# Optimization experiments

Hardware: AMD Instinct MI355X
Metric: run time of the kernel (lower is better)

The kernel has to match this reference:

```python
import jax, jax.numpy as jnp
import numpy as np

B, S, I, H = 32, 1024, 128, 128
D = 2 * H  # bidirectional concat feature dim


def setup_inputs() -> dict:
    key = jax.random.key(0)
    ks = jax.random.split(key, 12)
    lim = 1.0 / np.sqrt(H)  # PyTorch LSTMCell uniform init bound
    u = lambda k, shape: jax.random.uniform(k, shape, jnp.float32, -lim, lim)
    x = jax.random.normal(ks[0], (B, S, I), jnp.float32)
    return {
        "x": x,
        "fw_Wih": u(ks[1], (4 * H, I)), "fw_Whh": u(ks[2], (4 * H, H)),
        "fw_bih": u(ks[3], (4 * H,)),   "fw_bhh": u(ks[4], (4 * H,)),
        "bw_Wih": u(ks[5], (4 * H, I)), "bw_Whh": u(ks[6], (4 * H, H)),
        "bw_bih": u(ks[7], (4 * H,)),   "bw_bhh": u(ks[8], (4 * H,)),
        "Wq": u(ks[9], (D, D)), "Wk": u(ks[10], (D, D)), "Wv": u(ks[11], (D, D)),
    }


def _lstm_dir(x, Wih, Whh, bih, bhh):
    # x: [B, S, I] -> hidden states [B, S, H]; PyTorch LSTMCell gate math.
    xg = jnp.einsum('bsi,gi->bsg', x, Wih) + bih + bhh  # precompute input projections

    def step(carry, xg_t):
        h, c = carry
        g = xg_t + h @ Whh.T
        i_, f_, g_, o_ = jnp.split(g, 4, axis=-1)
        c = jax.nn.sigmoid(f_) * c + jax.nn.sigmoid(i_) * jnp.tanh(g_)
        h = jax.nn.sigmoid(o_) * jnp.tanh(c)
        return (h, c), h

    h0 = jnp.zeros((x.shape[0], Whh.shape[1]), x.dtype)
    _, hs = jax.lax.scan(step, (h0, h0), jnp.swapaxes(xg, 0, 1))
    return jnp.swapaxes(hs, 0, 1)


def reference(x, fw_Wih, fw_Whh, fw_bih, fw_bhh,
              bw_Wih, bw_Whh, bw_bih, bw_bhh, Wq, Wk, Wv):
    f_h = _lstm_dir(x, fw_Wih, fw_Whh, fw_bih, fw_bhh)            # [B,S,H]
    b_h = _lstm_dir(x[:, ::-1, :], bw_Wih, bw_Whh, bw_bih, bw_bhh)[:, ::-1, :]
    h = jnp.concatenate([f_h, b_h], axis=2)                        # [B,S,2H]
    q = h @ Wq.T
    k = h @ Wk.T
    v = h @ Wv.T
    att = jnp.einsum('bsd,btd->bst', q, k) / jnp.sqrt(jnp.asarray(D, h.dtype))
    att = jax.nn.softmax(att, axis=2)
    return jnp.einsum('bst,btd->bsd', att, v)
```

## Files before the change

kernel.cpp:

```cpp
#include <hip/hip_runtime.h>

typedef unsigned short u16;
typedef unsigned int u32;
typedef __bf16 bf16x8 __attribute__((ext_vector_type(8)));
typedef bf16x8 __attribute__((may_alias)) bf16x8a;
typedef float f32x4 __attribute__((ext_vector_type(4)));
typedef _Float16 f16;
typedef _Float16 f16x2 __attribute__((ext_vector_type(2)));

#define BB 32
#define SS 1024
#define HH 128
#define DD 256

__device__ __forceinline__ float b2f(u16 u) {
    u32 v = ((u32)u) << 16;
    return __builtin_bit_cast(float, v);
}
__device__ __forceinline__ u16 f2b(float f) {
    u32 u = __builtin_bit_cast(u32, f);
    u32 r = (u + 0x7fffu + ((u >> 16) & 1u)) >> 16;
    return (u16)r;
}
__device__ __forceinline__ float sig_fast(float x) {
    return __builtin_amdgcn_rcpf(1.0f + __builtin_amdgcn_exp2f(-1.4426950408889634f * x));
}
__device__ __forceinline__ float tanh_fast(float x) {
    return 2.0f * sig_fast(2.0f * x) - 1.0f;
}
template <int CTRL>
__device__ __forceinline__ float dpp_xor(float x) {
    return __builtin_bit_cast(float,
        __builtin_amdgcn_update_dpp(0, __builtin_bit_cast(int, x),
                                    CTRL, 0xF, 0xF, true));
}
__device__ __forceinline__ void lds_barrier() {
    asm volatile("s_waitcnt lgkmcnt(0)\n\ts_barrier" ::: "memory");
}

__global__ __launch_bounds__(256) void conv_weights(
    const float* __restrict__ fwWih, const float* __restrict__ bwWih,
    const float* __restrict__ fwWhh, const float* __restrict__ bwWhh,
    const float* __restrict__ Wq, const float* __restrict__ Wk,
    const float* __restrict__ Wv,
    u16* __restrict__ wfih, u16* __restrict__ wbih, u16* __restrict__ whhf,
    u16* __restrict__ wq, u16* __restrict__ wk, u16* __restrict__ wv)
{
    const int which = blockIdx.y;
    const float* src; u16* dst; int mode;
    switch (which) {
        case 0: src = fwWih; dst = wfih;              mode = 0; break;
        case 1: src = bwWih; dst = wbih;              mode = 0; break;
        case 2: src = fwWhh; dst = whhf;              mode = 1; break;
        case 3: src = bwWhh; dst = whhf + 512 * 128;  mode = 1; break;
        case 4: src = Wq;    dst = wq;                mode = 2; break;
        case 5: src = Wk;    dst = wk;                mode = 2; break;
        default: src = Wv;   dst = wv;                mode = 2; break;
    }
    for (int i = blockIdx.x * 256 + threadIdx.x; i < 65536 / 4; i += 32 * 256) {
        float4 v = ((const float4*)src)[i];
        ushort4 o;
        if (mode == 1) {
            o.x = __builtin_bit_cast(u16, (f16)v.x);
            o.y = __builtin_bit_cast(u16, (f16)v.y);
            o.z = __builtin_bit_cast(u16, (f16)v.z);
            o.w = __builtin_bit_cast(u16, (f16)v.w);
        } else {
            o.x = f2b(v.x); o.y = f2b(v.y); o.z = f2b(v.z); o.w = f2b(v.w);
        }
        if (mode == 2) {
            ((ushort4*)dst)[i] = o;
        } else {
            int r = i >> 5, c4 = i & 31;
            int rp = ((r & 127) << 2) | (r >> 7);
            *(ushort4*)&dst[rp * 128 + c4 * 4] = o;
        }
    }
}

template <int MODE, int AFP32>
__device__ __forceinline__ void gemm_core(
    const void* __restrict__ Araw, const u16* __restrict__ Bt,
    const float* __restrict__ bias1, const float* __restrict__ bias2,
    u16* __restrict__ Cout, int K, int N)
{
    __shared__ u16 As[128 * 72];
    __shared__ u16 Bs[128 * 72];
    const int tid = threadIdx.x;
    const int lane = tid & 63, wave = tid >> 6;
    const int wm = wave >> 1, wn = wave & 1;
    const int lo = lane & 15, hi = lane >> 4;
    const int m0 = blockIdx.x * 128, n0 = blockIdx.y * 128;

    f32x4 acc[4][4] = {};

    for (int k0 = 0; k0 < K; k0 += 64) {
        __syncthreads();
#pragma unroll
        for (int i = 0; i < 4; i++) {
            int c = tid + 256 * i;
            int row = c >> 3, kc = (c & 7) * 8;
            if (AFP32) {
                const float* ap = (const float*)Araw + (size_t)(m0 + row) * K + k0 + kc;
                float4 v0 = *(const float4*)ap;
                float4 v1 = *(const float4*)(ap + 4);
                uint4 o;
                o.x = (u32)f2b(v0.x) | ((u32)f2b(v0.y) << 16);
                o.y = (u32)f2b(v0.z) | ((u32)f2b(v0.w) << 16);
                o.z = (u32)f2b(v1.x) | ((u32)f2b(v1.y) << 16);
                o.w = (u32)f2b(v1.z) | ((u32)f2b(v1.w) << 16);
                *(uint4*)&As[row * 72 + kc] = o;
            } else {
                *(uint4*)&As[row * 72 + kc] =
                    *(const uint4*)&((const u16*)Araw)[(size_t)(m0 + row) * K + k0 + kc];
            }
            *(uint4*)&Bs[row * 72 + kc] =
                *(const uint4*)&Bt[(size_t)(n0 + row) * K + k0 + kc];
        }
        __syncthreads();
#pragma unroll
        for (int ks = 0; ks < 2; ks++) {
            bf16x8 af[4], bfr[4];
#pragma unroll
            for (int i = 0; i < 4; i++)
                af[i] = *(const bf16x8a*)&As[(wm * 64 + i * 16 + lo) * 72 + ks * 32 + hi * 8];
#pragma unroll
            for (int j = 0; j < 4; j++)
                bfr[j] = *(const bf16x8a*)&Bs[(wn * 64 + j * 16 + lo) * 72 + ks * 32 + hi * 8];
#pragma unroll
            for (int i = 0; i < 4; i++)
#pragma unroll
                for (int j = 0; j < 4; j++)
                    acc[i][j] = __builtin_amdgcn_mfma_f32_16x16x32_bf16(
                        af[i], bfr[j], acc[i][j], 0, 0, 0);
        }
    }
#pragma unroll
    for (int j = 0; j < 4; j++) {
        int col = n0 + wn * 64 + j * 16 + lo;
        float bsum = 0.f;
        if (MODE == 1) {
            int co = ((col & 3) << 7) | (col >> 2);
            bsum = bias1[co] + bias2[co];
        }
#pragma unroll
        for (int i = 0; i < 4; i++) {
            int row0 = m0 + wm * 64 + i * 16 + hi * 4;
#pragma unroll
            for (int r = 0; r < 4; r++) {
                float v = acc[i][j][r] + bsum;
                if (MODE == 1) {
                    int row = row0 + r;
                    int sidx = row & 1023, bidx = row >> 10;
                    Cout[(size_t)sidx * (BB * 512) + bidx * 512 + col] = f2b(v);
                } else {
                    Cout[(size_t)(row0 + r) * N + col] = f2b(v);
                }
            }
        }
    }
}

__global__ __launch_bounds__(256) void gemm_xg(
    const float* __restrict__ A, const u16* __restrict__ Bt_f,
    const u16* __restrict__ Bt_b,
    const float* __restrict__ f_bih, const float* __restrict__ f_bhh,
    const float* __restrict__ b_bih, const float* __restrict__ b_bhh,
    u16* __restrict__ xg)
{
    const int dir = blockIdx.z;
    gemm_core<1, 1>(A, dir ? Bt_b : Bt_f,
                    dir ? b_bih : f_bih, dir ? b_bhh : f_bhh,
                    xg + (size_t)dir * SS * BB * 512, 128, 512);
}

__global__ __launch_bounds__(256) void gemm_qkv(
    const u16* __restrict__ A, const u16* __restrict__ Wq,
    const u16* __restrict__ Wk, const u16* __restrict__ Wv,
    u16* __restrict__ qb, u16* __restrict__ kb, u16* __restrict__ vb)
{
    const int z = blockIdx.z;
    const u16* Bt = (z == 0) ? Wq : (z == 1) ? Wk : Wv;
    u16* out = (z == 0) ? qb : (z == 1) ? kb : vb;
    gemm_core<0, 0>(A, Bt, nullptr, nullptr, out, 256, 256);
}

__global__ __launch_bounds__(256)
__attribute__((amdgpu_waves_per_eu(1, 1)))
void lstm_scan_sk(
    const u16* __restrict__ Whh_h,
    const u16* __restrict__ xg,
    u16* __restrict__ hout)
{
    const int wg = blockIdx.x;
    const int dir = wg >> 5, b = wg & 31;
    const int t_ = threadIdx.x;
    const int u = t_ >> 1;
    const int kh = t_ & 1;

    u32 w[4][32];
    {
        const volatile u32* vp = (const volatile u32*)(Whh_h + (size_t)dir * 512 * 128);
#pragma unroll
        for (int g = 0; g < 4; g++) {
            int base = ((4 * u + g) * 128 + kh * 64) >> 1;
#pragma unroll
            for (int k = 0; k < 32; k++) w[g][k] = vp[base + k];
        }
    }

    __shared__ __align__(16) u16 hbuf[2][128];
    if (t_ < 128) hbuf[0][t_] = 0;
    float c = 0.0f;

    const u16* xgp = xg + (size_t)dir * SS * (BB * 512) + (size_t)b * 512 + 4 * u;
    u16* hop = hout + (size_t)b * SS * DD + dir * HH + u;

    int s = dir ? (SS - 1) : 0;
    const int d1 = dir ? -1 : 1;
    uint2 nxA = *(const uint2*)&xgp[(size_t)s * (BB * 512)];
    uint2 nxB = *(const uint2*)&xgp[(size_t)(s + d1) * (BB * 512)];
    lds_barrier();

    auto body = [&](uint2& nx, int parity) {
        uint2 xv = nx;
        int sp = s + 2 * d1;
        if ((unsigned)sp < SS)
            nx = *(const uint2*)&xgp[(size_t)sp * (BB * 512)];

        const uint4* hb = (const uint4*)&hbuf[parity][kh * 64];
        float g0 = 0.f, g1 = 0.f, g2 = 0.f, g3 = 0.f;
#pragma unroll
        for (int cc = 0; cc < 8; cc++) {
            uint4 hh = hb[cc];
            u32 hv[4] = {hh.x, hh.y, hh.z, hh.w};
#pragma unroll
            for (int j = 0; j < 4; j++) {
                f16x2 hp = __builtin_bit_cast(f16x2, hv[j]);
                g0 = __builtin_amdgcn_fdot2(hp, __builtin_bit_cast(f16x2, w[0][4 * cc + j]), g0, false);
                g1 = __builtin_amdgcn_fdot2(hp, __builtin_bit_cast(f16x2, w[1][4 * cc + j]), g1, false);
                g2 = __builtin_amdgcn_fdot2(hp, __builtin_bit_cast(f16x2, w[2][4 * cc + j]), g2, false);
                g3 = __builtin_amdgcn_fdot2(hp, __builtin_bit_cast(f16x2, w[3][4 * cc + j]), g3, false);
            }
        }
        g0 += dpp_xor<0xB1>(g0);
        g1 += dpp_xor<0xB1>(g1);
        g2 += dpp_xor<0xB1>(g2);
        g3 += dpp_xor<0xB1>(g3);
        g0 += b2f((u16)(xv.x & 0xffff)); g1 += b2f((u16)(xv.x >> 16));
        g2 += b2f((u16)(xv.y & 0xffff)); g3 += b2f((u16)(xv.y >> 16));

        c = fmaf(sig_fast(g1), c, sig_fast(g0) * tanh_fast(g2));
        float h = sig_fast(g3) * tanh_fast(c);

        if (kh == 0)
            hbuf[parity ^ 1][u] = __builtin_bit_cast(u16, (f16)h);
        else
            hop[(size_t)s * DD] = f2b(h);
        lds_barrier();
        s += d1;
    };

    for (int t = 0; t < SS; t += 2) {
        body(nxA, 0);
        body(nxB, 1);
    }
}

__global__ __launch_bounds__(256) void transpose_v(
    const u16* __restrict__ v, u16* __restrict__ vT)
{
    __shared__ u16 tile[64 * 72];
    const int b = blockIdx.z, s0 = blockIdx.x * 64, d0 = blockIdx.y * 64;
    const int tid = threadIdx.x;
#pragma unroll
    for (int i = 0; i < 2; i++) {
        int c = tid + 256 * i;
        int sl = c >> 3, dc = (c & 7) * 8;
        *(uint4*)&tile[sl * 72 + dc] =
            *(const uint4*)&v[((size_t)b * SS + s0 + sl) * DD + d0 + dc];
    }
    __syncthreads();
#pragma unroll
    for (int i = 0; i < 2; i++) {
        int c = tid + 256 * i;
        int dl = c >> 3, sc = (c & 7) * 8;
        u32 x0 = (u32)tile[(sc + 0) * 72 + dl] | ((u32)tile[(sc + 1) * 72 + dl] << 16);
        u32 x1 = (u32)tile[(sc + 2) * 72 + dl] | ((u32)tile[(sc + 3) * 72 + dl] << 16);
        u32 x2 = (u32)tile[(sc + 4) * 72 + dl] | ((u32)tile[(sc + 5) * 72 + dl] << 16);
        u32 x3 = (u32)tile[(sc + 6) * 72 + dl] | ((u32)tile[(sc + 7) * 72 + dl] << 16);
        uint4 val; val.x = x0; val.y = x1; val.z = x2; val.w = x3;
        *(uint4*)&vT[((size_t)b * DD + d0 + dl) * SS + s0 + sc] = val;
    }
}

__global__ __launch_bounds__(256) void attn_kernel(
    const u16* __restrict__ q, const u16* __restrict__ k,
    const u16* __restrict__ vT, float* __restrict__ out)
{
    __shared__ u16 Ks[32 * 264];
    __shared__ u16 Vs[256 * 40];
    __shared__ u16 Ps[64 * 40];
    const int b = blockIdx.y, q0 = blockIdx.x * 64;
    const int tid = threadIdx.x, wave = tid >> 6, lane = tid & 63;
    const int lo = lane & 15, hi = lane >> 4;
    const float c1 = 0.09016844005556021f;

    bf16x8 qf[8];
    {
        const u16* qp = q + ((size_t)b * SS + q0 + wave * 16 + lo) * DD;
#pragma unroll
        for (int ks = 0; ks < 8; ks++)
            qf[ks] = *(const bf16x8a*)&qp[ks * 32 + hi * 8];
    }
    float m_i[4] = {-1e30f, -1e30f, -1e30f, -1e30f};
    float l_i[4] = {0.f, 0.f, 0.f, 0.f};
    f32x4 o[16] = {};

    for (int t0 = 0; t0 < SS; t0 += 32) {
        __syncthreads();
#pragma unroll
        for (int i = 0; i < 4; i++) {
            int c = tid + 256 * i;
            {
                int row = c >> 5, dc = (c & 31) * 8;
                *(uint4*)&Ks[row * 264 + dc] =
                    *(const uint4*)&k[((size_t)b * SS + t0 + row) * DD + dc];
            }
            {
                int d = c >> 2, sc = (c & 3) * 8;
                *(uint4*)&Vs[d * 40 + sc] =
                    *(const uint4*)&vT[((size_t)b * DD + d) * SS + t0 + sc];
            }
        }
        __syncthreads();

        f32x4 sacc[2] = {};
#pragma unroll
        for (int ks = 0; ks < 8; ks++) {
#pragma unroll
            for (int j = 0; j < 2; j++) {
                bf16x8 bfr = *(const bf16x8a*)&Ks[(j * 16 + lo) * 264 + ks * 32 + hi * 8];
                sacc[j] = __builtin_amdgcn_mfma_f32_16x16x32_bf16(qf[ks], bfr, sacc[j], 0, 0, 0);
            }
        }

        float tt[2][4];
#pragma unroll
        for (int j = 0; j < 2; j++)
#pragma unroll
            for (int r = 0; r < 4; r++) tt[j][r] = sacc[j][r] * c1;
        float rm[4];
#pragma unroll
        for (int r = 0; r < 4; r++) rm[r] = fmaxf(tt[0][r], tt[1][r]);
#pragma unroll
        for (int mm = 1; mm <= 8; mm <<= 1)
#pragma unroll
            for (int r = 0; r < 4; r++) rm[r] = fmaxf(rm[r], __shfl_xor(rm[r], mm, 64));
        float al[4], rs[4];
#pragma unroll
        for (int r = 0; r < 4; r++) {
            float mn = fmaxf(m_i[r], rm[r]);
            al[r] = __builtin_amdgcn_exp2f(m_i[r] - mn);
            m_i[r] = mn;
            rs[r] = 0.f;
        }
#pragma unroll
        for (int j = 0; j < 2; j++)
#pragma unroll
            for (int r = 0; r < 4; r++) {
                float p = __builtin_amdgcn_exp2f(tt[j][r] - m_i[r]);
                rs[r] += p;
                Ps[(wave * 16 + hi * 4 + r) * 40 + j * 16 + lo] = f2b(p);
            }
#pragma unroll
        for (int mm = 1; mm <= 8; mm <<= 1)
#pragma unroll
            for (int r = 0; r < 4; r++) rs[r] += __shfl_xor(rs[r], mm, 64);
#pragma unroll
        for (int r = 0; r < 4; r++) l_i[r] = l_i[r] * al[r] + rs[r];
#pragma unroll
        for (int nt = 0; nt < 16; nt++) {
            o[nt][0] *= al[0]; o[nt][1] *= al[1];
            o[nt][2] *= al[2]; o[nt][3] *= al[3];
        }
        __syncthreads();
        bf16x8 pa = *(const bf16x8a*)&Ps[(wave * 16 + lo) * 40 + hi * 8];
#pragma unroll
        for (int nt = 0; nt < 16; nt++) {
            bf16x8 bv = *(const bf16x8a*)&Vs[(nt * 16 + lo) * 40 + hi * 8];
            o[nt] = __builtin_amdgcn_mfma_f32_16x16x32_bf16(pa, bv, o[nt], 0, 0, 0);
        }
    }
    float inv[4];
#pragma unroll
    for (int r = 0; r < 4; r++) inv[r] = __builtin_amdgcn_rcpf(l_i[r]);
#pragma unroll
    for (int nt = 0; nt < 16; nt++)
#pragma unroll
        for (int r = 0; r < 4; r++) {
            int row = q0 + wave * 16 + hi * 4 + r;
            int col = nt * 16 + lo;
            out[((size_t)b * SS + row) * DD + col] = o[nt][r] * inv[r];
        }
}

extern "C" void kernel_launch(void* const* d_in, const int* in_sizes, int n_in,
                              void* d_out, int out_size, void* d_ws, size_t ws_size,
                              hipStream_t stream)
{
    (void)in_sizes; (void)n_in; (void)out_size;
    const float* x      = (const float*)d_in[0];
    const float* fw_Wih = (const float*)d_in[1];
    const float* fw_Whh = (const float*)d_in[2];
    const float* fw_bih = (const float*)d_in[3];
    const float* fw_bhh = (const float*)d_in[4];
    const float* bw_Wih = (const float*)d_in[5];
    const float* bw_Whh = (const float*)d_in[6];
    const float* bw_bih = (const float*)d_in[7];
    const float* bw_bhh = (const float*)d_in[8];
    const float* Wq = (const float*)d_in[9];
    const float* Wk = (const float*)d_in[10];
    const float* Wv = (const float*)d_in[11];

    if (ws_size < 143523840ULL) return;

    char* ws = (char*)d_ws;
    u16* xg  = (u16*)ws;
    u16* h   = (u16*)(ws + 67108864);
    u16* qb  = (u16*)(ws + 83886080);
    u16* kb  = (u16*)(ws + 100663296);
    u16* vT  = (u16*)(ws + 117440512);
    u16* wfih16 = (u16*)(ws + 142606336);
    u16* wbih16 = (u16*)(ws + 142606336 + 131072);
    u16* wq16   = (u16*)(ws + 142606336 + 262144);
    u16* wk16   = (u16*)(ws + 142606336 + 393216);
    u16* wv16   = (u16*)(ws + 142606336 + 524288);
    u16* whhf16 = (u16*)(ws + 142606336 + 655360);
    u16* vb = (u16*)ws;

    conv_weights<<<dim3(32, 7), 256, 0, stream>>>(
        fw_Wih, bw_Wih, fw_Whh, bw_Whh, Wq, Wk, Wv,
        wfih16, wbih16, whhf16, wq16, wk16, wv16);

    gemm_xg<<<dim3(256, 4, 2), 256, 0, stream>>>(
        x, wfih16, wbih16, fw_bih, fw_bhh, bw_bih, bw_bhh, xg);
    lstm_scan_sk<<<64, 256, 0, stream>>>(whhf16, xg, h);
    gemm_qkv<<<dim3(256, 2, 3), 256, 0, stream>>>(h, wq16, wk16, wv16, qb, kb, vb);
    transpose_v<<<dim3(16, 4, 32), 256, 0, stream>>>(vb, vT);
    attn_kernel<<<dim3(16, 32), 256, 0, stream>>>(qb, kb, vT, (float*)d_out);
}
```

Before: 765.8 us.

## Process two batch rows per LSTM scan workgroup, halving the grid

Each LSTM scan workgroup now carries two independent batch sequences, reusing the register-resident Whh weights for both dot products and sharing one barrier per timestep. The grid shrinks from 64 to 32 workgroups. The aim is to give the serial, latency-bound recurrence more independent instructions per step to hide latency and to amortise barrier cost. In exchange, each step does twice the arithmetic and register pressure rises, and fewer CUs are used.

Result: slower. 1.150 ms (+50.2%).

```diff
diff --git a/kernel.cpp b/kernel.cpp
--- a/kernel.cpp
+++ b/kernel.cpp
@@ -193,7 +193,9 @@
     u16* __restrict__ hout)
 {
     const int wg = blockIdx.x;
-    const int dir = wg >> 5, b = wg & 31;
+    const int dir = wg >> 4;
+    const int bA = (wg & 15) * 2;
+    const int bB = bA + 1;
     const int t_ = threadIdx.x;
     const int u = t_ >> 1;
     const int kh = t_ & 1;
@@ -209,61 +211,87 @@
         }
     }
 
-    __shared__ __align__(16) u16 hbuf[2][128];
-    if (t_ < 128) hbuf[0][t_] = 0;
-    float c = 0.0f;
-
-    const u16* xgp = xg + (size_t)dir * SS * (BB * 512) + (size_t)b * 512 + 4 * u;
-    u16* hop = hout + (size_t)b * SS * DD + dir * HH + u;
+    __shared__ __align__(16) u16 hbuf[2][2][128];
+    if (t_ < 128) { hbuf[0][0][t_] = 0; hbuf[1][0][t_] = 0; }
+    float cA = 0.0f, cB = 0.0f;
+
+    const u16* xgpA = xg + (size_t)dir * SS * (BB * 512) + (size_t)bA * 512 + 4 * u;
+    const u16* xgpB = xg + (size_t)dir * SS * (BB * 512) + (size_t)bB * 512 + 4 * u;
+    u16* hopA = hout + (size_t)bA * SS * DD + dir * HH + u;
+    u16* hopB = hout + (size_t)bB * SS * DD + dir * HH + u;
 
     int s = dir ? (SS - 1) : 0;
     const int d1 = dir ? -1 : 1;
-    uint2 nxA = *(const uint2*)&xgp[(size_t)s * (BB * 512)];
-    uint2 nxB = *(const uint2*)&xgp[(size_t)(s + d1) * (BB * 512)];
+    uint2 nxA0 = *(const uint2*)&xgpA[(size_t)s * (BB * 512)];
+    uint2 nxB0 = *(const uint2*)&xgpB[(size_t)s * (BB * 512)];
+    uint2 nxA1 = *(const uint2*)&xgpA[(size_t)(s + d1) * (BB * 512)];
+    uint2 nxB1 = *(const uint2*)&xgpB[(size_t)(s + d1) * (BB * 512)];
     lds_barrier();
 
-    auto body = [&](uint2& nx, int parity) {
-        uint2 xv = nx;
+    auto body = [&](uint2& nxa, uint2& nxb, int parity) {
+        uint2 xva = nxa, xvb = nxb;
         int sp = s + 2 * d1;
-        if ((unsigned)sp < SS)
-            nx = *(const uint2*)&xgp[(size_t)sp * (BB * 512)];
-
-        const uint4* hb = (const uint4*)&hbuf[parity][kh * 64];
-        float g0 = 0.f, g1 = 0.f, g2 = 0.f, g3 = 0.f;
+        if ((unsigned)sp < SS) {
+            nxa = *(const uint2*)&xgpA[(size_t)sp * (BB * 512)];
+            nxb = *(const uint2*)&xgpB[(size_t)sp * (BB * 512)];
+        }
+
+        const uint4* hbA = (const uint4*)&hbuf[0][parity][kh * 64];
+        const uint4* hbB = (const uint4*)&hbuf[1][parity][kh * 64];
+        float a0 = 0.f, a1 = 0.f, a2 = 0.f, a3 = 0.f;
+        float b0 = 0.f, b1 = 0.f, b2 = 0.f, b3 = 0.f;
 #pragma unroll
         for (int cc = 0; cc < 8; cc++) {
-            uint4 hh = hb[cc];
-            u32 hv[4] = {hh.x, hh.y, hh.z, hh.w};
+            uint4 hhA = hbA[cc];
+            uint4 hhB = hbB[cc];
+            u32 hvA[4] = {hhA.x, hhA.y, hhA.z, hhA.w};
+            u32 hvB[4] = {hhB.x, hhB.y, hhB.z, hhB.w};
 #pragma unroll
             for (int j = 0; j < 4; j++) {
-                f16x2 hp = __builtin_bit_cast(f16x2, hv[j]);
-                g0 = __builtin_amdgcn_fdot2(hp, __builtin_bit_cast(f16x2, w[0][4 * cc + j]), g0, false);
-                g1 = __builtin_amdgcn_fdot2(hp, __builtin_bit_cast(f16x2, w[1][4 * cc + j]), g1, false);
-                g2 = __builtin_amdgcn_fdot2(hp, __builtin_bit_cast(f16x2, w[2][4 * cc + j]), g2, false);
-                g3 = __builtin_amdgcn_fdot2(hp, __builtin_bit_cast(f16x2, w[3][4 * cc + j]), g3, false);
-            }
-        }
-        g0 += dpp_xor<0xB1>(g0);
-        g1 += dpp_xor<0xB1>(g1);
-        g2 += dpp_xor<0xB1>(g2);
-        g3 += dpp_xor<0xB1>(g3);
-        g0 += b2f((u16)(xv.x & 0xffff)); g1 += b2f((u16)(xv.x >> 16));
-        g2 += b2f((u16)(xv.y & 0xffff)); g3 += b2f((u16)(xv.y >> 16));
-
-        c = fmaf(sig_fast(g1), c, sig_fast(g0) * tanh_fast(g2));
-        float h = sig_fast(g3) * tanh_fast(c);
-
-        if (kh == 0)
-            hbuf[parity ^ 1][u] = __builtin_bit_cast(u16, (f16)h);
-        else
-            hop[(size_t)s * DD] = f2b(h);
+                f16x2 wp0 = __builtin_bit_cast(f16x2, w[0][4 * cc + j]);
+                f16x2 wp1 = __builtin_bit_cast(f16x2, w[1][4 * cc + j]);
+                f16x2 wp2 = __builtin_bit_cast(f16x2, w[2][4 * cc + j]);
+                f16x2 wp3 = __builtin_bit_cast(f16x2, w[3][4 * cc + j]);
+                f16x2 hpA = __builtin_bit_cast(f16x2, hvA[j]);
+                f16x2 hpB = __builtin_bit_cast(f16x2, hvB[j]);
+                a0 = __builtin_amdgcn_fdot2(hpA, wp0, a0, false);
+                b0 = __builtin_amdgcn_fdot2(hpB, wp0, b0, false);
+                a1 = __builtin_amdgcn_fdot2(hpA, wp1, a1, false);
+                b1 = __builtin_amdgcn_fdot2(hpB, wp1, b1, false);
+                a2 = __builtin_amdgcn_fdot2(hpA, wp2, a2, false);
+                b2 = __builtin_amdgcn_fdot2(hpB, wp2, b2, false);
+                a3 = __builtin_amdgcn_fdot2(hpA, wp3, a3, false);
+                b3 = __builtin_amdgcn_fdot2(hpB, wp3, b3, false);
+            }
+        }
+        a0 += dpp_xor<0xB1>(a0); b0 += dpp_xor<0xB1>(b0);
+        a1 += dpp_xor<0xB1>(a1); b1 += dpp_xor<0xB1>(b1);
+        a2 += dpp_xor<0xB1>(a2); b2 += dpp_xor<0xB1>(b2);
+        a3 += dpp_xor<0xB1>(a3); b3 += dpp_xor<0xB1>(b3);
+        a0 += b2f((u16)(xva.x & 0xffff)); a1 += b2f((u16)(xva.x >> 16));
+        a2 += b2f((u16)(xva.y & 0xffff)); a3 += b2f((u16)(xva.y >> 16));
+        b0 += b2f((u16)(xvb.x & 0xffff)); b1 += b2f((u16)(xvb.x >> 16));
+        b2 += b2f((u16)(xvb.y & 0xffff)); b3 += b2f((u16)(xvb.y >> 16));
+
+        cA = fmaf(sig_fast(a1), cA, sig_fast(a0) * tanh_fast(a2));
+        cB = fmaf(sig_fast(b1), cB, sig_fast(b0) * tanh_fast(b2));
+        float hA = sig_fast(a3) * tanh_fast(cA);
+        float hB = sig_fast(b3) * tanh_fast(cB);
+
+        if (kh == 0) {
+            hbuf[0][parity ^ 1][u] = __builtin_bit_cast(u16, (f16)hA);
+            hbuf[1][parity ^ 1][u] = __builtin_bit_cast(u16, (f16)hB);
+        } else {
+            hopA[(size_t)s * DD] = f2b(hA);
+            hopB[(size_t)s * DD] = f2b(hB);
+        }
         lds_barrier();
         s += d1;
     };
 
     for (int t = 0; t < SS; t += 2) {
-        body(nxA, 0);
-        body(nxB, 1);
+        body(nxA0, nxB0, 0);
+        body(nxA1, nxB1, 1);
     }
 }
 
@@ -445,7 +473,7 @@
 
     gemm_xg<<<dim3(256, 4, 2), 256, 0, stream>>>(
         x, wfih16, wbih16, fw_bih, fw_bhh, bw_bih, bw_bhh, xg);
-    lstm_scan_sk<<<64, 256, 0, stream>>>(whhf16, xg, h);
+    lstm_scan_sk<<<32, 256, 0, stream>>>(whhf16, xg, h);
     gemm_qkv<<<dim3(256, 2, 3), 256, 0, stream>>>(h, wq16, wk16, wv16, qb, kb, vb);
     transpose_v<<<dim3(16, 4, 32), 256, 0, stream>>>(vb, vT);
     attn_kernel<<<dim3(16, 32), 256, 0, stream>>>(qb, kb, vT, (float*)d_out);
```

## Compute LSTM recurrent matvec with MFMA instead of per-thread fdot2

Applied to the files above, without the earlier changes.

The sequential LSTM scan now computes h·Whh^T with 16x16x32 f16 MFMA instructions. The broadcast hidden vector is loaded as the A operand, so only row 0 of each accumulator is used, and each wave owns 32 hidden units held as B-fragments in registers. This drops the long per-thread fdot2 chain and the DPP cross-lane reduction. The cost is 15/16 of the MFMA work being wasted and only 16 lanes per wave doing the gate math and the stores. The weight-conversion kernel also stops permuting Whh rows, to match the new fragment layout.

Result: slower. 880.1 us (+14.9%).

```diff
diff --git a/kernel.cpp b/kernel.cpp
--- a/kernel.cpp
+++ b/kernel.cpp
@@ -7,6 +7,7 @@
 typedef float f32x4 __attribute__((ext_vector_type(4)));
 typedef _Float16 f16;
 typedef _Float16 f16x2 __attribute__((ext_vector_type(2)));
+typedef _Float16 f16x8 __attribute__((ext_vector_type(8)));
 
 #define BB 32
 #define SS 1024
@@ -27,12 +28,6 @@
 }
 __device__ __forceinline__ float tanh_fast(float x) {
     return 2.0f * sig_fast(2.0f * x) - 1.0f;
-}
-template <int CTRL>
-__device__ __forceinline__ float dpp_xor(float x) {
-    return __builtin_bit_cast(float,
-        __builtin_amdgcn_update_dpp(0, __builtin_bit_cast(int, x),
-                                    CTRL, 0xF, 0xF, true));
 }
 __device__ __forceinline__ void lds_barrier() {
     asm volatile("s_waitcnt lgkmcnt(0)\n\ts_barrier" ::: "memory");
@@ -68,12 +63,12 @@
         } else {
             o.x = f2b(v.x); o.y = f2b(v.y); o.z = f2b(v.z); o.w = f2b(v.w);
         }
-        if (mode == 2) {
-            ((ushort4*)dst)[i] = o;
-        } else {
+        if (mode == 0) {
             int r = i >> 5, c4 = i & 31;
             int rp = ((r & 127) << 2) | (r >> 7);
             *(ushort4*)&dst[rp * 128 + c4 * 4] = o;
+        } else {
+            ((ushort4*)dst)[i] = o;
         }
     }
 }
@@ -195,75 +190,96 @@
     const int wg = blockIdx.x;
     const int dir = wg >> 5, b = wg & 31;
     const int t_ = threadIdx.x;
-    const int u = t_ >> 1;
-    const int kh = t_ & 1;
-
-    u32 w[4][32];
+    const int w = t_ >> 6;
+    const int lane = t_ & 63;
+    const int lo = lane & 15, hi = lane >> 4;
+
+    uint4 bfv[4][2][4];
     {
         const volatile u32* vp = (const volatile u32*)(Whh_h + (size_t)dir * 512 * 128);
 #pragma unroll
-        for (int g = 0; g < 4; g++) {
-            int base = ((4 * u + g) * 128 + kh * 64) >> 1;
-#pragma unroll
-            for (int k = 0; k < 32; k++) w[g][k] = vp[base + k];
-        }
+        for (int g = 0; g < 4; g++)
+#pragma unroll
+            for (int p = 0; p < 2; p++)
+#pragma unroll
+                for (int kt = 0; kt < 4; kt++) {
+                    int row = 16 * (2 * w + 8 * g + p) + lo;
+                    int base = (row * 128 + kt * 32 + hi * 8) >> 1;
+                    bfv[g][p][kt].x = vp[base + 0];
+                    bfv[g][p][kt].y = vp[base + 1];
+                    bfv[g][p][kt].z = vp[base + 2];
+                    bfv[g][p][kt].w = vp[base + 3];
+                }
     }
 
     __shared__ __align__(16) u16 hbuf[2][128];
     if (t_ < 128) hbuf[0][t_] = 0;
-    float c = 0.0f;
-
-    const u16* xgp = xg + (size_t)dir * SS * (BB * 512) + (size_t)b * 512 + 4 * u;
-    u16* hop = hout + (size_t)b * SS * DD + dir * HH + u;
+    float c0 = 0.0f, c1 = 0.0f;
+
+    const int u0 = 32 * w + lo;
+    const u16* xgp = xg + (size_t)dir * SS * (BB * 512) + (size_t)b * 512 + 4 * u0;
+    u16* hop = hout + (size_t)b * SS * DD + dir * HH + u0;
 
     int s = dir ? (SS - 1) : 0;
     const int d1 = dir ? -1 : 1;
-    uint2 nxA = *(const uint2*)&xgp[(size_t)s * (BB * 512)];
-    uint2 nxB = *(const uint2*)&xgp[(size_t)(s + d1) * (BB * 512)];
+    uint2 nxa0 = *(const uint2*)&xgp[(size_t)s * (BB * 512)];
+    uint2 nxb0 = *(const uint2*)&xgp[(size_t)s * (BB * 512) + 64];
+    uint2 nxa1 = *(const uint2*)&xgp[(size_t)(s + d1) * (BB * 512)];
+    uint2 nxb1 = *(const uint2*)&xgp[(size_t)(s + d1) * (BB * 512) + 64];
     lds_barrier();
 
-    auto body = [&](uint2& nx, int parity) {
-        uint2 xv = nx;
+    auto body = [&](uint2& nxa, uint2& nxb, int parity) {
+        uint2 xva = nxa, xvb = nxb;
         int sp = s + 2 * d1;
-        if ((unsigned)sp < SS)
-            nx = *(const uint2*)&xgp[(size_t)sp * (BB * 512)];
-
-        const uint4* hb = (const uint4*)&hbuf[parity][kh * 64];
-        float g0 = 0.f, g1 = 0.f, g2 = 0.f, g3 = 0.f;
-#pragma unroll
-        for (int cc = 0; cc < 8; cc++) {
-            uint4 hh = hb[cc];
-            u32 hv[4] = {hh.x, hh.y, hh.z, hh.w};
-#pragma unroll
-            for (int j = 0; j < 4; j++) {
-                f16x2 hp = __builtin_bit_cast(f16x2, hv[j]);
-                g0 = __builtin_amdgcn_fdot2(hp, __builtin_bit_cast(f16x2, w[0][4 * cc + j]), g0, false);
-                g1 = __builtin_amdgcn_fdot2(hp, __builtin_bit_cast(f16x2, w[1][4 * cc + j]), g1, false);
-                g2 = __builtin_amdgcn_fdot2(hp, __builtin_bit_cast(f16x2, w[2][4 * cc + j]), g2, false);
-                g3 = __builtin_amdgcn_fdot2(hp, __builtin_bit_cast(f16x2, w[3][4 * cc + j]), g3, false);
-            }
-        }
-        g0 += dpp_xor<0xB1>(g0);
-        g1 += dpp_xor<0xB1>(g1);
-        g2 += dpp_xor<0xB1>(g2);
-        g3 += dpp_xor<0xB1>(g3);
-        g0 += b2f((u16)(xv.x & 0xffff)); g1 += b2f((u16)(xv.x >> 16));
-        g2 += b2f((u16)(xv.y & 0xffff)); g3 += b2f((u16)(xv.y >> 16));
-
-        c = fmaf(sig_fast(g1), c, sig_fast(g0) * tanh_fast(g2));
-        float h = sig_fast(g3) * tanh_fast(c);
-
-        if (kh == 0)
-            hbuf[parity ^ 1][u] = __builtin_bit_cast(u16, (f16)h);
-        else
-            hop[(size_t)s * DD] = f2b(h);
+        if ((unsigned)sp < SS) {
+            nxa = *(const uint2*)&xgp[(size_t)sp * (BB * 512)];
+            nxb = *(const uint2*)&xgp[(size_t)sp * (BB * 512) + 64];
+        }
+
+        f16x8 af[4];
+#pragma unroll
+        for (int kt = 0; kt < 4; kt++)
+            af[kt] = __builtin_bit_cast(f16x8,
+                *(const uint4*)&hbuf[parity][kt * 32 + hi * 8]);
+
+        f32x4 acc[4][2] = {};
+#pragma unroll
+        for (int kt = 0; kt < 4; kt++)
+#pragma unroll
+            for (int g = 0; g < 4; g++)
+#pragma unroll
+                for (int p = 0; p < 2; p++)
+                    acc[g][p] = __builtin_amdgcn_mfma_f32_16x16x32_f16(
+                        af[kt], __builtin_bit_cast(f16x8, bfv[g][p][kt]),
+                        acc[g][p], 0, 0, 0);
+
+        float gi0 = acc[0][0][0] + b2f((u16)(xva.x & 0xffff));
+        float gf0 = acc[1][0][0] + b2f((u16)(xva.x >> 16));
+        float gg0 = acc[2][0][0] + b2f((u16)(xva.y & 0xffff));
+        float go0 = acc[3][0][0] + b2f((u16)(xva.y >> 16));
+        float gi1 = acc[0][1][0] + b2f((u16)(xvb.x & 0xffff));
+        float gf1 = acc[1][1][0] + b2f((u16)(xvb.x >> 16));
+        float gg1 = acc[2][1][0] + b2f((u16)(xvb.y & 0xffff));
+        float go1 = acc[3][1][0] + b2f((u16)(xvb.y >> 16));
+
+        c0 = fmaf(sig_fast(gf0), c0, sig_fast(gi0) * tanh_fast(gg0));
+        c1 = fmaf(sig_fast(gf1), c1, sig_fast(gi1) * tanh_fast(gg1));
+        float h0 = sig_fast(go0) * tanh_fast(c0);
+        float h1 = sig_fast(go1) * tanh_fast(c1);
+
+        if (lane < 16) {
+            hbuf[parity ^ 1][u0]      = __builtin_bit_cast(u16, (f16)h0);
+            hbuf[parity ^ 1][u0 + 16] = __builtin_bit_cast(u16, (f16)h1);
+            hop[(size_t)s * DD]      = f2b(h0);
+            hop[(size_t)s * DD + 16] = f2b(h1);
+        }
         lds_barrier();
         s += d1;
     };
 
     for (int t = 0; t < SS; t += 2) {
-        body(nxA, 0);
-        body(nxB, 1);
+        body(nxa0, nxb0, 0);
+        body(nxa1, nxb1, 1);
     }
 }
 
```
